# Optimization experiments

Hardware: AMD Instinct MI355X
Metric: run time of the kernel (lower is better)

## Reference

```python
import jax, jax.numpy as jnp
import numpy as np
from jax import lax

B, C, H, W = 4, 64, 64, 64
CH = C // 2  # edge_detect hidden channels
BN_EPS = 1e-5


def conv1x1(x, w, b):
    # x: (B,C,H,W), w: (O,C), b: (O,)
    return jnp.einsum('bchw,oc->bohw', x, w) + b[None, :, None, None]


def setup_inputs() -> dict:
    key = jax.random.key(0)
    ks = jax.random.split(key, 12)
    s = 1.0 / np.sqrt(C)
    inp = {
        'x': jax.random.normal(ks[0], (B, C, H, W), jnp.float32),
        'Wq': jax.random.normal(ks[1], (C, C), jnp.float32) * s,
        'bq': jnp.zeros((C,), jnp.float32),
        'Wk': jax.random.normal(ks[2], (C, C), jnp.float32) * s,
        'bk': jnp.zeros((C,), jnp.float32),
        'Wv': jax.random.normal(ks[3], (C, C), jnp.float32) * s,
        'bv': jnp.zeros((C,), jnp.float32),
        'We1': jax.random.normal(ks[4], (CH, C, 3, 3), jnp.float32) * (1.0 / np.sqrt(C * 9)),
        'be1': jnp.zeros((CH,), jnp.float32),
        'bn_w': jnp.ones((CH,), jnp.float32),
        'bn_b': jnp.zeros((CH,), jnp.float32),
        'bn_mean': jnp.zeros((CH,), jnp.float32),
        'bn_var': jnp.ones((CH,), jnp.float32),
        'We2': jax.random.normal(ks[5], (1, CH), jnp.float32) * (1.0 / np.sqrt(CH)),
        'be2': jnp.zeros((1,), jnp.float32),
        'gamma': jax.random.normal(ks[6], (1,), jnp.float32) * 0.1,
        'beta': jax.random.normal(ks[7], (1,), jnp.float32) * 0.1,
    }
    return inp


def reference(x, Wq, bq, Wk, bk, Wv, bv, We1, be1, bn_w, bn_b, bn_mean, bn_var, We2, be2, gamma, beta):
    b, c, h, w = x.shape
    hw = h * w
    q = conv1x1(x, Wq, bq).reshape(b, c, hw).transpose(0, 2, 1)  # (B,HW,C)
    k = conv1x1(x, Wk, bk).reshape(b, c, hw)                      # (B,C,HW)
    v = conv1x1(x, Wv, bv).reshape(b, c, hw)                      # (B,C,HW)

    energy = jnp.einsum('bnc,bcm->bnm', q, k)                      # (B,HW,HW)
    attention = jax.nn.softmax(energy, axis=-1)

    # edge_detect: 3x3 conv -> BN (eval stats) -> ReLU -> 1x1 conv -> sigmoid
    e = lax.conv_general_dilated(x, We1, (1, 1), 'SAME',
                                 dimension_numbers=('NCHW', 'OIHW', 'NCHW'))
    e = e + be1[None, :, None, None]
    e = (e - bn_mean[None, :, None, None]) * jax.lax.rsqrt(bn_var + BN_EPS)[None, :, None, None]
    e = e * bn_w[None, :, None, None] + bn_b[None, :, None, None]
    e = jax.nn.relu(e)
    e = conv1x1(e, We2, be2)                                       # (B,1,H,W)
    edge = jax.nn.sigmoid(e).reshape(b, 1, hw)                     # (B,1,HW)

    fa = attention * (1.0 + beta[0] * edge)                        # broadcast over query dim
    denom = jnp.maximum(jnp.sum(jnp.abs(fa), axis=2, keepdims=True), 1e-12)
    fa = fa / denom                                                # L1 renorm along keys

    out = jnp.einsum('bcm,bnm->bcn', v, fa).reshape(b, c, h, w)
    return gamma[0] * out + x
```

## Files before the change

### kernel.cpp

```cpp
#include <hip/hip_runtime.h>
#include <hip/hip_bf16.h>

typedef unsigned short u16;
typedef __attribute__((ext_vector_type(8))) __bf16 bf16x8;
typedef __attribute__((ext_vector_type(4))) float f32x4;
typedef __attribute__((ext_vector_type(16))) float f32x16;


#define NSPLIT 4

__device__ __forceinline__ u16 f2bf(float f) {
    unsigned u = __builtin_bit_cast(unsigned, f);
    u += 0x7FFFu + ((u >> 16) & 1u);
    return (u16)(u >> 16);
}
__device__ __forceinline__ float bf2f(u16 v) {
    unsigned u = ((unsigned)v) << 16;
    return __builtin_bit_cast(float, u);
}

__global__ __launch_bounds__(256) void qkv_edge_kernel(
    const float* __restrict__ x,
    const float* __restrict__ Wq, const float* __restrict__ bq,
    const float* __restrict__ Wk, const float* __restrict__ bk,
    const float* __restrict__ Wv, const float* __restrict__ bv,
    const float* __restrict__ We1, const float* __restrict__ be1,
    const float* __restrict__ bn_w, const float* __restrict__ bn_b,
    const float* __restrict__ bn_mean, const float* __restrict__ bn_var,
    const float* __restrict__ We2, const float* __restrict__ be2,
    const float* __restrict__ beta,
    u16* __restrict__ Qt, u16* __restrict__ Kt, u16* __restrict__ Vm,
    float* __restrict__ wkey)
{
    __shared__ __align__(16) u16 sm[33280];
    const int t = threadIdx.x;
    const int wv = t >> 6, lane = t & 63;
    const int quad = lane >> 4, l15 = lane & 15;

    if (blockIdx.x < 256) {
        u16* Wl   = sm;
        u16* xt_s = sm + 13824;
        u16* vt   = sm + 13824 + 4224;
        const int b = blockIdx.x >> 6;
        const int n0 = (blockIdx.x & 63) << 6;

        const float* Wmat[3] = {Wq, Wk, Wv};
#pragma unroll
        for (int m = 0; m < 3; ++m)
#pragma unroll
            for (int i = 0; i < 4; ++i) {
                int u = t + i * 256;
                float4 w4 = *reinterpret_cast<const float4*>(Wmat[m] + u * 4);
                int row = u >> 4, col = (u & 15) * 4;
                uint2 pk;
                pk.x = (unsigned)f2bf(w4.x) | ((unsigned)f2bf(w4.y) << 16);
                pk.y = (unsigned)f2bf(w4.z) | ((unsigned)f2bf(w4.w) << 16);
                *reinterpret_cast<uint2*>(&Wl[(m * 64 + row) * 72 + col]) = pk;
            }
        for (int i = 0; i < 16; ++i) {
            int lin = t + i * 256;
            int c = lin >> 6, nn = lin & 63;
            xt_s[nn * 66 + c] = f2bf(x[(size_t)(b * 64 + c) * 4096 + n0 + nn]);
        }
        __syncthreads();

        bf16x8 bx[2];
#pragma unroll
        for (int h = 0; h < 2; ++h)
            bx[h] = *reinterpret_cast<const bf16x8*>(
                &xt_s[(wv * 16 + l15) * 66 + h * 32 + quad * 8]);

        f32x4 d[3][4];
#pragma unroll
        for (int m = 0; m < 3; ++m)
#pragma unroll
            for (int mt = 0; mt < 4; ++mt) d[m][mt] = (f32x4){0.f, 0.f, 0.f, 0.f};

#pragma unroll
        for (int h = 0; h < 2; ++h)
#pragma unroll
            for (int m = 0; m < 3; ++m)
#pragma unroll
                for (int mt = 0; mt < 4; ++mt) {
                    bf16x8 af = *reinterpret_cast<const bf16x8*>(
                        &Wl[(m * 64 + mt * 16 + l15) * 72 + h * 32 + quad * 8]);
                    d[m][mt] = __builtin_amdgcn_mfma_f32_16x16x32_bf16(af, bx[h], d[m][mt], 0, 0, 0);
                }

        const float* bias[3] = {bq, bk, bv};
        const float L2E = 1.44269504f;
#pragma unroll
        for (int m = 0; m < 3; ++m)
#pragma unroll
            for (int mt = 0; mt < 4; ++mt) {
                float4 bi = *reinterpret_cast<const float4*>(bias[m] + mt * 16 + quad * 4);
                d[m][mt][0] += bi.x; d[m][mt][1] += bi.y; d[m][mt][2] += bi.z; d[m][mt][3] += bi.w;
                if (m == 0) {
                    d[m][mt][0] *= L2E; d[m][mt][1] *= L2E;
                    d[m][mt][2] *= L2E; d[m][mt][3] *= L2E;
                }
            }

        const int rowchunk = (n0 >> 4) + wv;
#pragma unroll
        for (int m = 0; m < 2; ++m) {
            u16* base = (m == 0 ? Qt : Kt) + (size_t)b * 262144;
#pragma unroll
            for (int mt = 0; mt < 4; ++mt) {
                uint2 pk;
                pk.x = (unsigned)f2bf(d[m][mt][0]) | ((unsigned)f2bf(d[m][mt][1]) << 16);
                pk.y = (unsigned)f2bf(d[m][mt][2]) | ((unsigned)f2bf(d[m][mt][3]) << 16);
                *reinterpret_cast<uint2*>(
                    base + ((size_t)(rowchunk * 8 + mt * 2 + (quad >> 1))) * 128 +
                    l15 * 8 + (quad & 1) * 4) = pk;
            }
        }
#pragma unroll
        for (int mt = 0; mt < 4; ++mt)
#pragma unroll
            for (int r = 0; r < 4; ++r)
                vt[(mt * 16 + quad * 4 + r) * 72 + wv * 16 + l15] = f2bf(d[2][mt][r]);
        __syncthreads();
        {
            u16* Vb_st = Vm + (size_t)b * 262144;
            const int kt = n0 >> 6;
#pragma unroll
            for (int i = 0; i < 2; ++i) {
                int unit = t + i * 256;
                int f = unit >> 7, hq = (unit >> 4) & 7, cl = unit & 15;
                const u16* src = &vt[(f * 16 + cl) * 72 + hq * 8];
                uint4 v4 = *reinterpret_cast<const uint4*>(src);
                *reinterpret_cast<uint4*>(
                    Vb_st + ((size_t)((kt * 4 + f) * 8 + hq)) * 128 + cl * 8) = v4;
            }
        }
    } else {
        u16* Ae_s = sm;
        u16* xr_s = sm + 18688;
        const int eb = blockIdx.x - 256;
        const int b = eb >> 6, h = eb & 63;

        if (t < 192) {
            int kh = t / 64, rem = t & 63;
            int col = (rem >> 5) * 65, ci2 = (rem & 31) * 2;
            *reinterpret_cast<unsigned*>(&xr_s[(kh * 66 + col) * 72 + ci2]) = 0u;
        }
#pragma unroll
        for (int i = 0; i < 18; ++i) {
            int u = t + i * 256;
            int ch = u / 144;
            int rem = u - ch * 144;
            int p = rem >> 4, cig = (rem & 15) * 4;
            const float* src = We1 + ch * 576 + cig * 9 + p;
            float a = src[0], b2 = src[9], c2 = src[18], d2 = src[27];
            uint2 pk;
            pk.x = (unsigned)f2bf(a) | ((unsigned)f2bf(b2) << 16);
            pk.y = (unsigned)f2bf(c2) | ((unsigned)f2bf(d2) << 16);
            *reinterpret_cast<uint2*>(&Ae_s[ch * 584 + p * 64 + cig]) = pk;
        }
#pragma unroll
        for (int i = 0; i < 12; ++i) {
            int u = t + i * 256;
            int w = u & 63, cig = (u >> 6) & 15, kh = u >> 10;
            int hs = h + kh - 1;
            float v0 = 0.f, v1 = 0.f, v2 = 0.f, v3 = 0.f;
            if ((unsigned)hs < 64u) {
                const float* src = x + ((size_t)(b * 64 + cig * 4) * 64 + hs) * 64 + w;
                v0 = src[0]; v1 = src[4096]; v2 = src[8192]; v3 = src[12288];
            }
            uint2 pk;
            pk.x = (unsigned)f2bf(v0) | ((unsigned)f2bf(v1) << 16);
            pk.y = (unsigned)f2bf(v2) | ((unsigned)f2bf(v3) << 16);
            *reinterpret_cast<uint2*>(&xr_s[(kh * 66 + w + 1) * 72 + cig * 4]) = pk;
        }
        __syncthreads();

        f32x4 e[2];
        e[0] = (f32x4){0.f, 0.f, 0.f, 0.f};
        e[1] = (f32x4){0.f, 0.f, 0.f, 0.f};
#pragma unroll
        for (int p = 0; p < 9; ++p) {
            const int kh = p / 3, kw = p - kh * 3;
#pragma unroll
            for (int half = 0; half < 2; ++half) {
                bf16x8 bfr = *reinterpret_cast<const bf16x8*>(
                    &xr_s[(kh * 66 + wv * 16 + l15 + kw) * 72 + half * 32 + quad * 8]);
#pragma unroll
                for (int mt = 0; mt < 2; ++mt) {
                    bf16x8 af = *reinterpret_cast<const bf16x8*>(
                        &Ae_s[(mt * 16 + l15) * 584 + p * 64 + half * 32 + quad * 8]);
                    e[mt] = __builtin_amdgcn_mfma_f32_16x16x32_bf16(af, bfr, e[mt], 0, 0, 0);
                }
            }
        }
        float partial = 0.f;
#pragma unroll
        for (int mt = 0; mt < 2; ++mt) {
            float4 bw = *reinterpret_cast<const float4*>(bn_w    + mt * 16 + quad * 4);
            float4 bb = *reinterpret_cast<const float4*>(bn_b    + mt * 16 + quad * 4);
            float4 bm = *reinterpret_cast<const float4*>(bn_mean + mt * 16 + quad * 4);
            float4 bv2 = *reinterpret_cast<const float4*>(bn_var + mt * 16 + quad * 4);
            float4 b1 = *reinterpret_cast<const float4*>(be1     + mt * 16 + quad * 4);
            float4 w2 = *reinterpret_cast<const float4*>(We2     + mt * 16 + quad * 4);
            float sc, sh;
            sc = bw.x * rsqrtf(bv2.x + 1e-5f); sh = (b1.x - bm.x) * sc + bb.x;
            partial += fmaxf(e[mt][0] * sc + sh, 0.f) * w2.x;
            sc = bw.y * rsqrtf(bv2.y + 1e-5f); sh = (b1.y - bm.y) * sc + bb.y;
            partial += fmaxf(e[mt][1] * sc + sh, 0.f) * w2.y;
            sc = bw.z * rsqrtf(bv2.z + 1e-5f); sh = (b1.z - bm.z) * sc + bb.z;
            partial += fmaxf(e[mt][2] * sc + sh, 0.f) * w2.z;
            sc = bw.w * rsqrtf(bv2.w + 1e-5f); sh = (b1.w - bm.w) * sc + bb.w;
            partial += fmaxf(e[mt][3] * sc + sh, 0.f) * w2.w;
        }
        partial += __shfl_xor(partial, 16);
        partial += __shfl_xor(partial, 32);
        if (lane < 16) {
            float s = partial + be2[0];
            float sg = 1.f / (1.f + __expf(-s));
            wkey[(size_t)b * 4096 + h * 64 + wv * 16 + lane] =
                __log2f(fmaxf(1.f + beta[0] * sg, 1e-20f)) - 17.3123405f;
        }
    }
}

__global__ __launch_bounds__(256, 2) void attn_kernel(
    const u16* __restrict__ Qt, const u16* __restrict__ Kt,
    const u16* __restrict__ Vm, const float* __restrict__ lwkey,
    u16* __restrict__ O_part, float* __restrict__ l_part)
{
    constexpr int KT_ITERS = 64 / NSPLIT;
    const int t = threadIdx.x;
    const int qi = blockIdx.x / NSPLIT;
    const int split = blockIdx.x % NSPLIT;
    const int b = qi >> 5;
    const int n0 = (qi & 31) << 7;
    const int wv = t >> 6, lane = t & 63;
    const int l31 = lane & 31, hi = lane >> 5;
    const int i4 = (lane >> 4) & 1, l15 = lane & 15;

    const u16* Qb = Qt + (size_t)b * 262144;
    const u16* Kb = Kt + (size_t)b * 262144;
    const u16* Vb = Vm + (size_t)b * 262144;
    const float* lwb = lwkey + (size_t)b * 4096;

    bf16x8 qf[4];
#pragma unroll
    for (int kc = 0; kc < 4; ++kc)
        qf[kc] = __builtin_bit_cast(bf16x8, *reinterpret_cast<const uint4*>(
            Qb + (size_t)(((n0 >> 4) + wv * 2 + i4) * 8 + kc * 2 + hi) * 128 + l15 * 8));

    const int kt0 = split * KT_ITERS;
    uint4 kf[2][4];
#pragma unroll
    for (int tl = 0; tl < 2; ++tl)
#pragma unroll
        for (int kc = 0; kc < 4; ++kc)
            kf[tl][kc] = *reinterpret_cast<const uint4*>(
                Kb + (size_t)((kt0 * 4 + tl * 2 + i4) * 8 + kc * 2 + hi) * 128 + l15 * 8);

    f32x16 o[2];
#pragma unroll
    for (int ct = 0; ct < 2; ++ct)
#pragma unroll
        for (int i = 0; i < 16; ++i) o[ct][i] = 0.f;
    float lacc0 = 0.f, lacc1 = 0.f;

    for (int kt = kt0; kt < kt0 + KT_ITERS; ++kt) {
        uint4 vf[2][4];
#pragma unroll
        for (int ct = 0; ct < 2; ++ct)
#pragma unroll
            for (int kc = 0; kc < 4; ++kc)
                vf[ct][kc] = *reinterpret_cast<const uint4*>(
                    Vb + (size_t)((kt * 4 + ct * 2 + i4) * 8 + kc * 2 + hi) * 128 + l15 * 8);

        float4 lwv[2][4];
#pragma unroll
        for (int tl = 0; tl < 2; ++tl)
#pragma unroll
            for (int g = 0; g < 4; ++g)
                lwv[tl][g] = *reinterpret_cast<const float4*>(
                    lwb + kt * 64 + tl * 32 + g * 8 + hi * 4);

        f32x16 s[2];
#pragma unroll
        for (int tl = 0; tl < 2; ++tl) {
            f32x16 a;
#pragma unroll
            for (int i = 0; i < 16; ++i) a[i] = 0.f;
#pragma unroll
            for (int kc = 0; kc < 4; ++kc)
                a = __builtin_amdgcn_mfma_f32_32x32x16_bf16(
                        __builtin_bit_cast(bf16x8, kf[tl][kc]), qf[kc], a, 0, 0, 0);
            s[tl] = a;
        }

        const int ktn = (kt + 1 < kt0 + KT_ITERS) ? kt + 1 : kt0;
#pragma unroll
        for (int tl = 0; tl < 2; ++tl)
#pragma unroll
            for (int kc = 0; kc < 4; ++kc)
                kf[tl][kc] = *reinterpret_cast<const uint4*>(
                    Kb + (size_t)((ktn * 4 + tl * 2 + i4) * 8 + kc * 2 + hi) * 128 + l15 * 8);

        uint4 pb[2][2];
#pragma unroll
        for (int tl = 0; tl < 2; ++tl) {
            float p[16];
#pragma unroll
            for (int g = 0; g < 4; ++g) {
                const float4 lv = lwv[tl][g];
                p[4 * g + 0] = exp2f(s[tl][4 * g + 0] + lv.x);
                p[4 * g + 1] = exp2f(s[tl][4 * g + 1] + lv.y);
                p[4 * g + 2] = exp2f(s[tl][4 * g + 2] + lv.z);
                p[4 * g + 3] = exp2f(s[tl][4 * g + 3] + lv.w);
                lacc0 += p[4 * g + 0] + p[4 * g + 1];
                lacc1 += p[4 * g + 2] + p[4 * g + 3];
            }
#pragma unroll
            for (int kc2 = 0; kc2 < 2; ++kc2) {
                int a0, a1, b0, b1;
                asm("v_cvt_pk_bf16_f32 %0, %1, %2" : "=v"(a0) : "v"(p[kc2 * 8 + 0]), "v"(p[kc2 * 8 + 1]));
                asm("v_cvt_pk_bf16_f32 %0, %1, %2" : "=v"(a1) : "v"(p[kc2 * 8 + 2]), "v"(p[kc2 * 8 + 3]));
                asm("v_cvt_pk_bf16_f32 %0, %1, %2" : "=v"(b0) : "v"(p[kc2 * 8 + 4]), "v"(p[kc2 * 8 + 5]));
                asm("v_cvt_pk_bf16_f32 %0, %1, %2" : "=v"(b1) : "v"(p[kc2 * 8 + 6]), "v"(p[kc2 * 8 + 7]));
                auto swA = __builtin_amdgcn_permlane32_swap(a0, b0, false, false);
                auto swB = __builtin_amdgcn_permlane32_swap(a1, b1, false, false);
                uint4 fr;
                fr.x = (unsigned)swA[0];
                fr.y = (unsigned)swB[0];
                fr.z = (unsigned)swA[1];
                fr.w = (unsigned)swB[1];
                pb[tl][kc2] = fr;
            }
        }

#pragma unroll
        for (int ct = 0; ct < 2; ++ct)
#pragma unroll
            for (int tl = 0; tl < 2; ++tl)
#pragma unroll
                for (int kc2 = 0; kc2 < 2; ++kc2)
                    o[ct] = __builtin_amdgcn_mfma_f32_32x32x16_bf16(
                        __builtin_bit_cast(bf16x8, vf[ct][tl * 2 + kc2]),
                        __builtin_bit_cast(bf16x8, pb[tl][kc2]), o[ct], 0, 0, 0);
    }

    float lh = lacc0 + lacc1;
    float ltot = lh + __shfl_xor(lh, 32);
    if (lane < 32)
        l_part[(size_t)blockIdx.x * 128 + wv * 32 + lane] = ltot;

    const size_t pbase = (size_t)blockIdx.x * 8192;
    const int q = wv * 32 + l31;
#pragma unroll
    for (int ct = 0; ct < 2; ++ct)
#pragma unroll
        for (int g = 0; g < 4; ++g) {
            int w0, w1;
            asm("v_cvt_pk_bf16_f32 %0, %1, %2" : "=v"(w0) : "v"(o[ct][4 * g + 0]), "v"(o[ct][4 * g + 1]));
            asm("v_cvt_pk_bf16_f32 %0, %1, %2" : "=v"(w1) : "v"(o[ct][4 * g + 2]), "v"(o[ct][4 * g + 3]));
            uint2 pk2;
            pk2.x = (unsigned)w0;
            pk2.y = (unsigned)w1;
            *reinterpret_cast<uint2*>(
                &O_part[pbase + (size_t)(ct * 8 + g * 2 + hi) * 512 + q * 4]) = pk2;
        }
}

__global__ __launch_bounds__(256) void combine_kernel(
    const u16* __restrict__ O_part, const float* __restrict__ l_part,
    const float* __restrict__ x, const float* __restrict__ g_gamma,
    float* __restrict__ out)
{
    __shared__ float ot[32 * 65];
    __shared__ float ls[32];
    const int t = threadIdx.x;
    const int ab = blockIdx.x >> 2;
    const int sub = blockIdx.x & 3;
    const int b = ab >> 5;
    const int n0 = (ab & 31) << 7;
    const float gamma = g_gamma[0];

#pragma unroll
    for (int i = 0; i < 2; ++i) {
        int idx = t + i * 256;
        int c4 = idx >> 5, ql = idx & 31;
        float a0 = 0.f, a1 = 0.f, a2 = 0.f, a3 = 0.f;
#pragma unroll
        for (int s4 = 0; s4 < NSPLIT; ++s4) {
            uint2 u = *reinterpret_cast<const uint2*>(
                O_part + ((size_t)(ab * NSPLIT + s4)) * 8192 +
                (size_t)c4 * 512 + (sub * 32 + ql) * 4);
            a0 += bf2f((u16)(u.x & 0xFFFF));
            a1 += bf2f((u16)(u.x >> 16));
            a2 += bf2f((u16)(u.y & 0xFFFF));
            a3 += bf2f((u16)(u.y >> 16));
        }
        ot[ql * 65 + c4 * 4 + 0] = a0;
        ot[ql * 65 + c4 * 4 + 1] = a1;
        ot[ql * 65 + c4 * 4 + 2] = a2;
        ot[ql * 65 + c4 * 4 + 3] = a3;
    }
    if (t < 32) {
        float lsum = 0.f;
#pragma unroll
        for (int s4 = 0; s4 < NSPLIT; ++s4)
            lsum += l_part[((size_t)(ab * NSPLIT + s4)) * 128 + sub * 32 + t];
        ls[t] = gamma / fmaxf(lsum, 1e-30f);
    }
    __syncthreads();
    {
        const int c = t >> 2, seg = t & 3;
        const size_t gbase = ((size_t)(b * 64 + c)) * 4096 + n0 + sub * 32 + seg * 8;
#pragma unroll
        for (int j = 0; j < 2; ++j) {
            float4 xv = *reinterpret_cast<const float4*>(&x[gbase + j * 4]);
            float4 rv;
            int nl = seg * 8 + j * 4;
            rv.x = ot[(nl + 0) * 65 + c] * ls[nl + 0] + xv.x;
            rv.y = ot[(nl + 1) * 65 + c] * ls[nl + 1] + xv.y;
            rv.z = ot[(nl + 2) * 65 + c] * ls[nl + 2] + xv.z;
            rv.w = ot[(nl + 3) * 65 + c] * ls[nl + 3] + xv.w;
            *reinterpret_cast<float4*>(&out[gbase + j * 4]) = rv;
        }
    }
}

extern "C" void kernel_launch(void* const* d_in, const int* in_sizes, int n_in,
                              void* d_out, int out_size, void* d_ws, size_t ws_size,
                              hipStream_t stream) {
    const float* x      = (const float*)d_in[0];
    const float* Wq     = (const float*)d_in[1];
    const float* bq     = (const float*)d_in[2];
    const float* Wk     = (const float*)d_in[3];
    const float* bk     = (const float*)d_in[4];
    const float* Wv     = (const float*)d_in[5];
    const float* bv     = (const float*)d_in[6];
    const float* We1    = (const float*)d_in[7];
    const float* be1    = (const float*)d_in[8];
    const float* bn_w   = (const float*)d_in[9];
    const float* bn_b   = (const float*)d_in[10];
    const float* bn_mean= (const float*)d_in[11];
    const float* bn_var = (const float*)d_in[12];
    const float* We2    = (const float*)d_in[13];
    const float* be2    = (const float*)d_in[14];
    const float* gamma  = (const float*)d_in[15];
    const float* beta   = (const float*)d_in[16];

    char* ws = (char*)d_ws;
    const size_t KB = 1024, MB = 1024 * 1024;
    u16*   Qt     = (u16*)ws;
    u16*   Kt     = (u16*)(ws + 2 * MB);
    u16*   Vm     = (u16*)(ws + 4 * MB);
    float* lw     = (float*)(ws + 6 * MB);
    float* l_part = (float*)(ws + 6 * MB + 64 * KB);
    u16*   O_part = (u16*)(ws + 6 * MB + 576 * KB);

    float* out = (float*)d_out;

    qkv_edge_kernel<<<dim3(512), dim3(256), 0, stream>>>(
        x, Wq, bq, Wk, bk, Wv, bv, We1, be1, bn_w, bn_b, bn_mean, bn_var,
        We2, be2, beta, Qt, Kt, Vm, lw);
    attn_kernel<<<dim3(128 * NSPLIT), dim3(256), 0, stream>>>(
        Qt, Kt, Vm, lw, O_part, l_part);
    combine_kernel<<<dim3(512), dim3(256), 0, stream>>>(
        O_part, l_part, x, gamma, out);
}
```

Before: 156.4 us.

## Double key splits, remap block order, and restructure attention inner loop

Raises the key-dimension split count from 4 to 8 so more blocks run in parallel. Blocks are remapped so that consecutive block IDs go to different query tiles, spreading work across XCDs and improving cache locality. The K register prefetch is dropped in favour of per-tile loads through precomputed advancing pointers, and the MFMA sections are wrapped in s_setprio. More splits double the partial-output traffic and the combine work, and removing the prefetch may expose load latency.

```diff
diff --git a/kernel.cpp b/kernel.cpp
--- a/kernel.cpp
+++ b/kernel.cpp
@@ -7,7 +7,7 @@
 typedef __attribute__((ext_vector_type(16))) float f32x16;
 
 
-#define NSPLIT 4
+#define NSPLIT 8
 
 __device__ __forceinline__ u16 f2bf(float f) {
     unsigned u = __builtin_bit_cast(unsigned, f);
@@ -229,94 +229,73 @@
     u16* __restrict__ O_part, float* __restrict__ l_part)
 {
     constexpr int KT_ITERS = 64 / NSPLIT;
+    const int bid = ((blockIdx.x & 7) << 7) + (blockIdx.x >> 3);
     const int t = threadIdx.x;
-    const int qi = blockIdx.x / NSPLIT;
-    const int split = blockIdx.x % NSPLIT;
+    const int qi = bid / NSPLIT;
+    const int split = bid % NSPLIT;
     const int b = qi >> 5;
     const int n0 = (qi & 31) << 7;
     const int wv = t >> 6, lane = t & 63;
     const int l31 = lane & 31, hi = lane >> 5;
     const int i4 = (lane >> 4) & 1, l15 = lane & 15;
 
+    const int kvoff = i4 * 1024 + hi * 128 + l15 * 8;
     const u16* Qb = Qt + (size_t)b * 262144;
-    const u16* Kb = Kt + (size_t)b * 262144;
-    const u16* Vb = Vm + (size_t)b * 262144;
-    const float* lwb = lwkey + (size_t)b * 4096;
+    const u16* Kp = Kt + (size_t)b * 262144 + (size_t)(split * KT_ITERS) * 4096 + kvoff;
+    const u16* Vp = Vm + (size_t)b * 262144 + (size_t)(split * KT_ITERS) * 4096 + kvoff;
+    const float* lwp = lwkey + (size_t)b * 4096 + (split * KT_ITERS) * 64 + hi * 4;
 
     bf16x8 qf[4];
 #pragma unroll
     for (int kc = 0; kc < 4; ++kc)
         qf[kc] = __builtin_bit_cast(bf16x8, *reinterpret_cast<const uint4*>(
-            Qb + (size_t)(((n0 >> 4) + wv * 2 + i4) * 8 + kc * 2 + hi) * 128 + l15 * 8));
-
-    const int kt0 = split * KT_ITERS;
-    uint4 kf[2][4];
-#pragma unroll
-    for (int tl = 0; tl < 2; ++tl)
-#pragma unroll
-        for (int kc = 0; kc < 4; ++kc)
-            kf[tl][kc] = *reinterpret_cast<const uint4*>(
-                Kb + (size_t)((kt0 * 4 + tl * 2 + i4) * 8 + kc * 2 + hi) * 128 + l15 * 8);
+            Qb + (size_t)(((n0 >> 4) + wv * 2) * 1024) + kvoff + kc * 256));
 
     f32x16 o[2];
 #pragma unroll
     for (int ct = 0; ct < 2; ++ct)
 #pragma unroll
         for (int i = 0; i < 16; ++i) o[ct][i] = 0.f;
-    float lacc0 = 0.f, lacc1 = 0.f;
-
-    for (int kt = kt0; kt < kt0 + KT_ITERS; ++kt) {
-        uint4 vf[2][4];
-#pragma unroll
-        for (int ct = 0; ct < 2; ++ct)
-#pragma unroll
-            for (int kc = 0; kc < 4; ++kc)
-                vf[ct][kc] = *reinterpret_cast<const uint4*>(
-                    Vb + (size_t)((kt * 4 + ct * 2 + i4) * 8 + kc * 2 + hi) * 128 + l15 * 8);
-
-        float4 lwv[2][4];
-#pragma unroll
-        for (int tl = 0; tl < 2; ++tl)
-#pragma unroll
-            for (int g = 0; g < 4; ++g)
-                lwv[tl][g] = *reinterpret_cast<const float4*>(
-                    lwb + kt * 64 + tl * 32 + g * 8 + hi * 4);
-
-        f32x16 s[2];
+    float lacc = 0.f;
+
+    for (int kt = 0; kt < KT_ITERS; ++kt) {
+        uint4 pbu[2][2];
 #pragma unroll
         for (int tl = 0; tl < 2; ++tl) {
-            f32x16 a;
-#pragma unroll
-            for (int i = 0; i < 16; ++i) a[i] = 0.f;
-#pragma unroll
-            for (int kc = 0; kc < 4; ++kc)
-                a = __builtin_amdgcn_mfma_f32_32x32x16_bf16(
-                        __builtin_bit_cast(bf16x8, kf[tl][kc]), qf[kc], a, 0, 0, 0);
-            s[tl] = a;
-        }
-
-        const int ktn = (kt + 1 < kt0 + KT_ITERS) ? kt + 1 : kt0;
-#pragma unroll
-        for (int tl = 0; tl < 2; ++tl)
-#pragma unroll
-            for (int kc = 0; kc < 4; ++kc)
-                kf[tl][kc] = *reinterpret_cast<const uint4*>(
-                    Kb + (size_t)((ktn * 4 + tl * 2 + i4) * 8 + kc * 2 + hi) * 128 + l15 * 8);
-
-        uint4 pb[2][2];
-#pragma unroll
-        for (int tl = 0; tl < 2; ++tl) {
+            uint4 k0 = *reinterpret_cast<const uint4*>(Kp + tl * 2048);
+            uint4 k1 = *reinterpret_cast<const uint4*>(Kp + tl * 2048 + 256);
+            uint4 k2 = *reinterpret_cast<const uint4*>(Kp + tl * 2048 + 512);
+            uint4 k3 = *reinterpret_cast<const uint4*>(Kp + tl * 2048 + 768);
+            float4 lw0 = *reinterpret_cast<const float4*>(lwp + tl * 32);
+            float4 lw1 = *reinterpret_cast<const float4*>(lwp + tl * 32 + 8);
+            float4 lw2 = *reinterpret_cast<const float4*>(lwp + tl * 32 + 16);
+            float4 lw3 = *reinterpret_cast<const float4*>(lwp + tl * 32 + 24);
+
+            f32x16 s;
+#pragma unroll
+            for (int i = 0; i < 16; ++i) s[i] = 0.f;
+            __builtin_amdgcn_s_setprio(1);
+            s = __builtin_amdgcn_mfma_f32_32x32x16_bf16(__builtin_bit_cast(bf16x8, k0), qf[0], s, 0, 0, 0);
+            s = __builtin_amdgcn_mfma_f32_32x32x16_bf16(__builtin_bit_cast(bf16x8, k1), qf[1], s, 0, 0, 0);
+            s = __builtin_amdgcn_mfma_f32_32x32x16_bf16(__builtin_bit_cast(bf16x8, k2), qf[2], s, 0, 0, 0);
+            s = __builtin_amdgcn_mfma_f32_32x32x16_bf16(__builtin_bit_cast(bf16x8, k3), qf[3], s, 0, 0, 0);
+            __builtin_amdgcn_s_setprio(0);
+
             float p[16];
-#pragma unroll
-            for (int g = 0; g < 4; ++g) {
-                const float4 lv = lwv[tl][g];
-                p[4 * g + 0] = exp2f(s[tl][4 * g + 0] + lv.x);
-                p[4 * g + 1] = exp2f(s[tl][4 * g + 1] + lv.y);
-                p[4 * g + 2] = exp2f(s[tl][4 * g + 2] + lv.z);
-                p[4 * g + 3] = exp2f(s[tl][4 * g + 3] + lv.w);
-                lacc0 += p[4 * g + 0] + p[4 * g + 1];
-                lacc1 += p[4 * g + 2] + p[4 * g + 3];
-            }
+            p[0]  = exp2f(s[0]  + lw0.x); p[1]  = exp2f(s[1]  + lw0.y);
+            p[2]  = exp2f(s[2]  + lw0.z); p[3]  = exp2f(s[3]  + lw0.w);
+            p[4]  = exp2f(s[4]  + lw1.x); p[5]  = exp2f(s[5]  + lw1.y);
+            p[6]  = exp2f(s[6]  + lw1.z); p[7]  = exp2f(s[7]  + lw1.w);
+            p[8]  = exp2f(s[8]  + lw2.x); p[9]  = exp2f(s[9]  + lw2.y);
+            p[10] = exp2f(s[10] + lw2.z); p[11] = exp2f(s[11] + lw2.w);
+            p[12] = exp2f(s[12] + lw3.x); p[13] = exp2f(s[13] + lw3.y);
+            p[14] = exp2f(s[14] + lw3.z); p[15] = exp2f(s[15] + lw3.w);
+            float t0 = (p[0] + p[1]) + (p[2] + p[3]);
+            float t1 = (p[4] + p[5]) + (p[6] + p[7]);
+            float t2 = (p[8] + p[9]) + (p[10] + p[11]);
+            float t3 = (p[12] + p[13]) + (p[14] + p[15]);
+            lacc += (t0 + t1) + (t2 + t3);
+
 #pragma unroll
             for (int kc2 = 0; kc2 < 2; ++kc2) {
                 int a0, a1, b0, b1;
@@ -331,27 +310,35 @@
                 fr.y = (unsigned)swB[0];
                 fr.z = (unsigned)swA[1];
                 fr.w = (unsigned)swB[1];
-                pb[tl][kc2] = fr;
-            }
-        }
-
-#pragma unroll
-        for (int ct = 0; ct < 2; ++ct)
-#pragma unroll
-            for (int tl = 0; tl < 2; ++tl)
-#pragma unroll
-                for (int kc2 = 0; kc2 < 2; ++kc2)
-                    o[ct] = __builtin_amdgcn_mfma_f32_32x32x16_bf16(
-                        __builtin_bit_cast(bf16x8, vf[ct][tl * 2 + kc2]),
-                        __builtin_bit_cast(bf16x8, pb[tl][kc2]), o[ct], 0, 0, 0);
+                pbu[tl][kc2] = fr;
+            }
+        }
+
+#pragma unroll
+        for (int ct = 0; ct < 2; ++ct) {
+            uint4 v0 = *reinterpret_cast<const uint4*>(Vp + ct * 2048);
+            uint4 v1 = *reinterpret_cast<const uint4*>(Vp + ct * 2048 + 256);
+            uint4 v2 = *reinterpret_cast<const uint4*>(Vp + ct * 2048 + 512);
+            uint4 v3 = *reinterpret_cast<const uint4*>(Vp + ct * 2048 + 768);
+            __builtin_amdgcn_s_setprio(1);
+            o[ct] = __builtin_amdgcn_mfma_f32_32x32x16_bf16(__builtin_bit_cast(bf16x8, v0),
+                        __builtin_bit_cast(bf16x8, pbu[0][0]), o[ct], 0, 0, 0);
+            o[ct] = __builtin_amdgcn_mfma_f32_32x32x16_bf16(__builtin_bit_cast(bf16x8, v1),
+                        __builtin_bit_cast(bf16x8, pbu[0][1]), o[ct], 0, 0, 0);
+            o[ct] = __builtin_amdgcn_mfma_f32_32x32x16_bf16(__builtin_bit_cast(bf16x8, v2),
+                        __builtin_bit_cast(bf16x8, pbu[1][0]), o[ct], 0, 0, 0);
+            o[ct] = __builtin_amdgcn_mfma_f32_32x32x16_bf16(__builtin_bit_cast(bf16x8, v3),
+                        __builtin_bit_cast(bf16x8, pbu[1][1]), o[ct], 0, 0, 0);
+            __builtin_amdgcn_s_setprio(0);
+        }
+        Kp += 4096; Vp += 4096; lwp += 64;
     }
 
-    float lh = lacc0 + lacc1;
-    float ltot = lh + __shfl_xor(lh, 32);
+    float ltot = lacc + __shfl_xor(lacc, 32);
     if (lane < 32)
-        l_part[(size_t)blockIdx.x * 128 + wv * 32 + lane] = ltot;
-
-    const size_t pbase = (size_t)blockIdx.x * 8192;
+        l_part[(size_t)bid * 128 + wv * 32 + lane] = ltot;
+
+    const size_t pbase = (size_t)bid * 8192;
     const int q = wv * 32 + l31;
 #pragma unroll
     for (int ct = 0; ct < 2; ++ct)
```

Measured after the change: 136.9 us. 12.5% less time.
